# Kernel tuning notes

Measured on AMD Instinct MI355X. Metric: run time of the kernel, lower is better.

Reference implementation:

```python
import jax, jax.numpy as jnp
import numpy as np

D_MODEL = 1024
NUM_LAYERS = 4
VOCAB = 32000
NUM_HEADS = 8
HEAD_DIM = D_MODEL // NUM_HEADS
FFN_DIM = 2048
BATCH = 4
SEQ = 1024
LN_EPS = 1e-5
ROPE_THETA = 10000.0


def setup_inputs() -> dict:
    key = jax.random.key(0)
    ks = iter(jax.random.split(key, 32))
    std = 0.02
    L, D, H, Dh, F, V = NUM_LAYERS, D_MODEL, NUM_HEADS, HEAD_DIM, FFN_DIM, VOCAB
    inp = {
        "tokens": jax.random.randint(next(ks), (BATCH, SEQ), 0, V, dtype=jnp.int32),
        "emb": jax.random.normal(next(ks), (V, D), jnp.float32),
        # per-layer stacked params; Linear weights stored pre-transposed (in, out)
        "Wqkv": jax.random.normal(next(ks), (L, D, 3 * D), jnp.float32) * std,
        "bqkv": jnp.zeros((L, 3 * D), jnp.float32),
        "Wo": jax.random.normal(next(ks), (L, D, D), jnp.float32) * std,
        "bo": jnp.zeros((L, D), jnp.float32),
        "ln1_g": jnp.ones((L, D), jnp.float32),
        "ln1_b": jnp.zeros((L, D), jnp.float32),
        "ln2_g": jnp.ones((L, D), jnp.float32),
        "ln2_b": jnp.zeros((L, D), jnp.float32),
        "W1": jax.random.normal(next(ks), (L, D, F), jnp.float32) * std,
        "b1": jnp.zeros((L, F), jnp.float32),
        "W2": jax.random.normal(next(ks), (L, F, D), jnp.float32) * std,
        "b2": jnp.zeros((L, D), jnp.float32),
        "lnf_g": jnp.ones((D,), jnp.float32),
        "lnf_b": jnp.zeros((D,), jnp.float32),
        "Wout": jax.random.normal(next(ks), (D, V), jnp.float32) * std,
        "bout": jnp.zeros((V,), jnp.float32),
    }
    return inp


def _layernorm(x, g, b):
    mu = jnp.mean(x, -1, keepdims=True)
    var = jnp.mean(jnp.square(x - mu), -1, keepdims=True)
    return (x - mu) * jax.lax.rsqrt(var + LN_EPS) * g + b


def _rope_cos_sin(seq, dh, dtype):
    inv_freq = 1.0 / (ROPE_THETA ** (jnp.arange(0, dh, 2, dtype=jnp.float32) / dh))
    t = jnp.arange(seq, dtype=jnp.float32)
    freqs = jnp.outer(t, inv_freq)                      # [S, Dh/2]
    emb = jnp.concatenate([freqs, freqs], axis=-1)      # [S, Dh]
    return jnp.cos(emb).astype(dtype), jnp.sin(emb).astype(dtype)


def _rotate_half(x):
    x1, x2 = jnp.split(x, 2, axis=-1)
    return jnp.concatenate([-x2, x1], axis=-1)


def _apply_rope(x, cos, sin):
    # x: [B,S,H,Dh]; cos/sin: [S,Dh] -> broadcast over batch and heads
    return x * cos[None, :, None, :] + _rotate_half(x) * sin[None, :, None, :]


def reference(tokens, emb, Wqkv, bqkv, Wo, bo, ln1_g, ln1_b, ln2_g, ln2_b,
              W1, b1, W2, b2, lnf_g, lnf_b, Wout, bout):
    B, S = tokens.shape
    H, Dh = NUM_HEADS, HEAD_DIM
    x = emb[tokens]                                      # [B,S,D]
    cos, sin = _rope_cos_sin(S, Dh, x.dtype)
    causal = jnp.tril(jnp.ones((S, S), dtype=bool))      # True = keep
    scale = 1.0 / jnp.sqrt(jnp.asarray(Dh, x.dtype))

    def layer(xc, p):
        (wqkv, bq, wo, bo_, g1, b1_, g2, b2_, w1, bb1, w2, bb2) = p
        y = _layernorm(xc, g1, b1_)
        qkv = (y @ wqkv + bq).reshape(B, S, 3, H, Dh)
        q, k, v = qkv[:, :, 0], qkv[:, :, 1], qkv[:, :, 2]
        q = _apply_rope(q, cos, sin)
        k = _apply_rope(k, cos, sin)
        scores = jnp.einsum("bshd,bthd->bhst", q, k) * scale
        scores = jnp.where(causal[None, None], scores, -jnp.inf)
        attn = jax.nn.softmax(scores, axis=-1)
        ctx = jnp.einsum("bhst,bthd->bshd", attn, v).reshape(B, S, H * Dh)
        xc = xc + ctx @ wo + bo_
        z = _layernorm(xc, g2, b2_)
        ff = jax.nn.gelu(z @ w1 + bb1, approximate=False) @ w2 + bb2
        return xc + ff, None

    params = (Wqkv, bqkv, Wo, bo, ln1_g, ln1_b, ln2_g, ln2_b, W1, b1, W2, b2)
    x, _ = jax.lax.scan(layer, x, params)
    x = _layernorm(x, lnf_g, lnf_b)
    return x @ Wout + bout                                # [B,S,V]
```

## Files before the change

### kernel.cpp

```cpp
#include <hip/hip_runtime.h>
#include <hip/hip_bf16.h>
#include <math.h>


#define D_MODEL 1024
#define SEQ     1024
#define BATCH   4
#define NHEAD   8
#define HDIM    128
#define FFN     2048
#define NLAYER  4
#define VOCAB   32000
#define MROWS   (BATCH*SEQ)

typedef unsigned short ushort_t;
typedef __attribute__((ext_vector_type(8))) short s16x8;
typedef __attribute__((ext_vector_type(4))) float f32x4;

__device__ __forceinline__ ushort_t f2bf(float f) {
    union { float f; unsigned int u; } c; c.f = f;
    unsigned int u = c.u;
    unsigned int r = (u + 0x7FFFu + ((u >> 16) & 1u)) >> 16;
    return (ushort_t)r;
}
__device__ __forceinline__ float bf2f(ushort_t u) {
    union { unsigned int u; float f; } c; c.u = ((unsigned int)u) << 16; return c.f;
}

__device__ __forceinline__ void gload16(const void* g, void* l) {
    __builtin_amdgcn_global_load_lds(
        (const __attribute__((address_space(1))) unsigned int*)g,
        (__attribute__((address_space(3))) unsigned int*)l, 16, 0, 0);
}

__global__ __launch_bounds__(256) void embed_kernel(
    const int* __restrict__ tokens, const float* __restrict__ emb,
    float* __restrict__ X)
{
    int row = blockIdx.x;
    int t = tokens[row];
    const float4* src = (const float4*)(emb + (size_t)t * D_MODEL);
    float4* dst = (float4*)(X + (size_t)row * D_MODEL);
    dst[threadIdx.x] = src[threadIdx.x];
}

__global__ __launch_bounds__(256) void ln_kernel(
    const float* __restrict__ X, const float* __restrict__ g,
    const float* __restrict__ b, ushort_t* __restrict__ Y)
{
    __shared__ float red[8];
    int row = blockIdx.x;
    const float4* x4 = (const float4*)(X + (size_t)row * D_MODEL);
    float4 v = x4[threadIdx.x];
    float s  = v.x + v.y + v.z + v.w;
    float ss = v.x*v.x + v.y*v.y + v.z*v.z + v.w*v.w;
    #pragma unroll
    for (int o = 32; o > 0; o >>= 1) { s += __shfl_down(s, o); ss += __shfl_down(ss, o); }
    int wid = threadIdx.x >> 6;
    if ((threadIdx.x & 63) == 0) { red[wid] = s; red[wid + 4] = ss; }
    __syncthreads();
    float tot  = red[0] + red[1] + red[2] + red[3];
    float tot2 = red[4] + red[5] + red[6] + red[7];
    float mu  = tot * (1.0f / D_MODEL);
    float var = tot2 * (1.0f / D_MODEL) - mu * mu;
    float r = rsqrtf(var + 1e-5f);
    const float4* g4 = (const float4*)g;
    const float4* b4 = (const float4*)b;
    float4 gv = g4[threadIdx.x], bv = b4[threadIdx.x];
    ushort4 o;
    o.x = f2bf((v.x - mu) * r * gv.x + bv.x);
    o.y = f2bf((v.y - mu) * r * gv.y + bv.y);
    o.z = f2bf((v.z - mu) * r * gv.z + bv.z);
    o.w = f2bf((v.w - mu) * r * gv.w + bv.w);
    ((ushort4*)(Y + (size_t)row * D_MODEL))[threadIdx.x] = o;
}

__global__ __launch_bounds__(256) void wconv(
    const float* __restrict__ W, ushort_t* __restrict__ Wt, int K, int N)
{
    __shared__ float t[32][33];
    const float* Wl = W + (size_t)blockIdx.z * K * N;
    ushort_t* Wtl = Wt + (size_t)blockIdx.z * K * N;
    int k0 = blockIdx.y * 32, n0 = blockIdx.x * 32;
    int tid = threadIdx.x;
    int r = tid >> 3, c4 = (tid & 7) * 4;
    float4 v = *(const float4*)(Wl + (size_t)(k0 + r) * N + n0 + c4);
    t[r][c4+0] = v.x; t[r][c4+1] = v.y; t[r][c4+2] = v.z; t[r][c4+3] = v.w;
    __syncthreads();
    ushort4 o;
    o.x = f2bf(t[c4+0][r]); o.y = f2bf(t[c4+1][r]);
    o.z = f2bf(t[c4+2][r]); o.w = f2bf(t[c4+3][r]);
    *(ushort4*)(Wtl + (size_t)(n0 + r) * K + k0 + c4) = o;
}

__device__ __forceinline__ float gelu_exact(float x) {
    return 0.5f * x * (1.0f + erff(x * 0.70710678118654752f));
}

template<int ACT, int BETA, int OBF>
__global__ __launch_bounds__(256) void gemm_mfma(
    const ushort_t* __restrict__ A, const ushort_t* __restrict__ Bt,
    const float* __restrict__ bias, float* __restrict__ Cf,
    ushort_t* __restrict__ Cb, int M, int N, int K)
{
    __shared__ __align__(16) ushort_t As[128 * 32];
    __shared__ __align__(16) ushort_t Bs[128 * 32];
    int tid  = threadIdx.x;
    int lane = tid & 63, w = tid >> 6;
    int wr = w >> 1, wc = w & 1;
    int m0 = blockIdx.x * 128, n0 = blockIdx.y * 128;

    f32x4 acc[4][4] = {};

    const ushort_t* gA = A  + (size_t)(m0 + w * 32 + (lane >> 2)) * K + (lane & 3) * 8;
    const ushort_t* gB = Bt + (size_t)(n0 + w * 32 + (lane >> 2)) * K + (lane & 3) * 8;
    ushort_t* lA = As + w * 1024;
    ushort_t* lB = Bs + w * 1024;
    const size_t gstep16 = (size_t)16 * K;

    int lrow = lane & 15, kg = lane >> 4;
    const s16x8* pa = (const s16x8*)(As + (wr * 64 + lrow) * 32 + kg * 8);
    const s16x8* pb = (const s16x8*)(Bs + (wc * 64 + lrow) * 32 + kg * 8);

    for (int kt = 0; kt < K / 32; ++kt) {
        gload16(gA, lA);
        gload16(gA + gstep16, lA + 512);
        gload16(gB, lB);
        gload16(gB + gstep16, lB + 512);
        gA += 32; gB += 32;
        __syncthreads();
        s16x8 a[4], b[4];
        #pragma unroll
        for (int mi = 0; mi < 4; ++mi) a[mi] = pa[mi * 64];
        #pragma unroll
        for (int ni = 0; ni < 4; ++ni) b[ni] = pb[ni * 64];
        #pragma unroll
        for (int mi = 0; mi < 4; ++mi)
            #pragma unroll
            for (int ni = 0; ni < 4; ++ni)
                acc[mi][ni] = __builtin_amdgcn_mfma_f32_16x16x32_bf16(
                    a[mi], b[ni], acc[mi][ni], 0, 0, 0);
        __syncthreads();
    }

    #pragma unroll
    for (int mi = 0; mi < 4; ++mi) {
        int rbase = m0 + wr * 64 + mi * 16 + (lane >> 4) * 4;
        #pragma unroll
        for (int ni = 0; ni < 4; ++ni) {
            int col = n0 + wc * 64 + ni * 16 + (lane & 15);
            float bz = bias[col];
            f32x4 v = acc[mi][ni];
            #pragma unroll
            for (int j = 0; j < 4; ++j) {
                float x = v[j] + bz;
                if (ACT == 1) x = gelu_exact(x);
                size_t off = (size_t)(rbase + j) * N + col;
                if (OBF) {
                    Cb[off] = f2bf(x);
                } else {
                    if (BETA) x += Cf[off];
                    Cf[off] = x;
                }
            }
        }
    }
}

__global__ __launch_bounds__(64) void rope_table_kernel(float2* __restrict__ RT)
{
    int s = blockIdx.x, p = threadIdx.x;
    float inv = expf(-0.14391156831212788f * (float)p);
    float ang = (float)s * inv;
    float sn, c;
    sincosf(ang, &sn, &c);
    RT[s * 64 + p] = make_float2(c, sn);
}

__global__ __launch_bounds__(256) void ropeq_kernel(
    const ushort_t* __restrict__ QKVb, const float2* __restrict__ RT,
    ushort_t* __restrict__ Qb, ushort_t* __restrict__ Kb)
{
    int m = blockIdx.x;
    int b = m >> 10, s = m & (SEQ - 1);
    const ushort_t* rowbase = QKVb + (size_t)m * (3 * D_MODEL);
    const float2* t2 = RT + s * 64;
    int tid = threadIdx.x;
    int qk = tid >> 7;
    int rem = tid & 127;
    int hh = rem >> 4;
    int p4 = (rem & 15) * 4;
    const ushort_t* base = rowbase + qk * D_MODEL + hh * HDIM + p4;
    ushort4 lo = *(const ushort4*)base;
    ushort4 hi = *(const ushort4*)(base + 64);
    ushort_t lov[4] = {lo.x, lo.y, lo.z, lo.w};
    ushort_t hiv[4] = {hi.x, hi.y, hi.z, hi.w};
    ushort_t lor[4], hir[4];
    #pragma unroll
    for (int j = 0; j < 4; ++j) {
        float2 cs = t2[p4 + j];
        float x1 = bf2f(lov[j]), x2 = bf2f(hiv[j]);
        lor[j] = f2bf(x1 * cs.x - x2 * cs.y);
        hir[j] = f2bf(x2 * cs.x + x1 * cs.y);
    }
    ushort_t* dst = (qk ? Kb : Qb) + ((size_t)(b * NHEAD + hh) * SEQ + s) * HDIM + p4;
    *(ushort4*)dst        = make_ushort4(lor[0], lor[1], lor[2], lor[3]);
    *(ushort4*)(dst + 64) = make_ushort4(hir[0], hir[1], hir[2], hir[3]);
}

__global__ __launch_bounds__(256) void vtrans_kernel(
    const ushort_t* __restrict__ QKVb, ushort_t* __restrict__ Vt)
{
    __shared__ ushort_t tl[64][34];
    int s0 = blockIdx.x * 64;
    int d0 = blockIdx.y * 32;
    int b  = blockIdx.z;
    int tid = threadIdx.x;
    #pragma unroll
    for (int r = 0; r < 4; ++r) {
        int li = tid + r * 256;
        int row = li >> 4;
        int cp  = (li & 15) * 2;
        ushort2 v = *(const ushort2*)(QKVb + (size_t)(b * SEQ + s0 + row) * 3072
                                      + 2 * D_MODEL + d0 + cp);
        tl[row][cp]     = v.x;
        tl[row][cp + 1] = v.y;
    }
    __syncthreads();
    #pragma unroll
    for (int r = 0; r < 4; ++r) {
        int li = tid + r * 256;
        int drow = li >> 5;
        int sc   = (li & 31) * 2;
        ushort2 o;
        o.x = tl[sc][drow];
        o.y = tl[sc + 1][drow];
        *(ushort2*)(Vt + (size_t)(b * D_MODEL + d0 + drow) * SEQ + s0 + sc) = o;
    }
}

#define PSTR 72

__global__ __launch_bounds__(256) void attn_mfma(
    const ushort_t* __restrict__ Qb, const ushort_t* __restrict__ Kb,
    const ushort_t* __restrict__ Vt, ushort_t* __restrict__ Yb)
{
    __shared__ __align__(16) ushort_t Ks[64 * 136];
    __shared__ __align__(16) ushort_t Vts[128 * 72];
    __shared__ __align__(16) ushort_t Pl[4][16 * PSTR];
    int bid = blockIdx.x;
    int qt = bid & 15, h = (bid >> 4) & 7, b = bid >> 7;
    int q0 = qt * 64;
    int tid = threadIdx.x, lane = tid & 63, w = tid >> 6;
    int lr = lane & 15, g = lane >> 4;
    const float scale = 0.08838834764831845f;

    const ushort_t* Qbase = Qb + (size_t)((b * NHEAD + h) * SEQ) * HDIM;
    const ushort_t* Kbase = Kb + (size_t)((b * NHEAD + h) * SEQ) * HDIM;
    const ushort_t* Vbase = Vt + (size_t)(b * D_MODEL + h * HDIM) * SEQ;

    s16x8 aq[4];
    #pragma unroll
    for (int kc = 0; kc < 4; ++kc)
        aq[kc] = *(const s16x8*)(Qbase + (size_t)(q0 + w * 16 + lr) * HDIM + kc * 32 + g * 8);

    f32x4 acc_o[8] = {};
    float mx[4] = {-INFINITY, -INFINITY, -INFINITY, -INFINITY};
    float ls[4] = {};

    int ntiles = q0 / 64 + 1;
    for (int t = 0; t < ntiles; ++t) {
        int j0 = t * 64;
        __syncthreads();
        #pragma unroll
        for (int r = 0; r < 4; ++r) {
            int idx = tid + r * 256;
            int row = idx >> 4, c16 = idx & 15;
            *(s16x8*)&Ks[row * 136 + c16 * 8] =
                *(const s16x8*)(Kbase + (size_t)(j0 + row) * HDIM + c16 * 8);
        }
        #pragma unroll
        for (int r = 0; r < 4; ++r) {
            int idx = tid + r * 256;
            int row = idx >> 3, c8 = idx & 7;
            *(s16x8*)&Vts[row * 72 + c8 * 8] =
                *(const s16x8*)(Vbase + (size_t)row * SEQ + j0 + c8 * 8);
        }
        __syncthreads();

        f32x4 sa[4] = {};
        __builtin_amdgcn_s_setprio(1);
        #pragma unroll
        for (int nb = 0; nb < 4; ++nb)
            #pragma unroll
            for (int kc = 0; kc < 4; ++kc) {
                s16x8 bk = *(const s16x8*)&Ks[(nb * 16 + lr) * 136 + kc * 32 + g * 8];
                sa[nb] = __builtin_amdgcn_mfma_f32_16x16x32_bf16(aq[kc], bk, sa[nb], 0, 0, 0);
            }
        __builtin_amdgcn_s_setprio(0);

        bool diag = (j0 == q0);
        float pv[4][4];
        #pragma unroll
        for (int nb = 0; nb < 4; ++nb)
            #pragma unroll
            for (int j = 0; j < 4; ++j) {
                float v = sa[nb][j] * scale;
                if (diag) {
                    int kv = j0 + nb * 16 + lr;
                    int qq = q0 + w * 16 + g * 4 + j;
                    if (kv > qq) v = -INFINITY;
                }
                pv[nb][j] = v;
            }
        #pragma unroll
        for (int j = 0; j < 4; ++j) {
            float tm = fmaxf(fmaxf(pv[0][j], pv[1][j]), fmaxf(pv[2][j], pv[3][j]));
            #pragma unroll
            for (int o = 1; o < 16; o <<= 1) tm = fmaxf(tm, __shfl_xor(tm, o));
            float nm = fmaxf(mx[j], tm);
            float corr = expf(mx[j] - nm);
            float ts = 0.0f;
            #pragma unroll
            for (int nb = 0; nb < 4; ++nb) {
                float e = expf(pv[nb][j] - nm);
                pv[nb][j] = e;
                ts += e;
            }
            #pragma unroll
            for (int o = 1; o < 16; o <<= 1) ts += __shfl_xor(ts, o);
            ls[j] = ls[j] * corr + ts;
            mx[j] = nm;
            #pragma unroll
            for (int dn = 0; dn < 8; ++dn) acc_o[dn][j] *= corr;
        }
        #pragma unroll
        for (int nb = 0; nb < 4; ++nb)
            #pragma unroll
            for (int j = 0; j < 4; ++j)
                Pl[w][(g * 4 + j) * PSTR + nb * 16 + lr] = f2bf(pv[nb][j]);
        #pragma unroll
        for (int kk = 0; kk < 2; ++kk) {
            s16x8 pa = *(const s16x8*)&Pl[w][lr * PSTR + kk * 32 + g * 8];
            __builtin_amdgcn_s_setprio(1);
            #pragma unroll
            for (int dn = 0; dn < 8; ++dn) {
                s16x8 bv = *(const s16x8*)&Vts[(dn * 16 + lr) * 72 + kk * 32 + g * 8];
                acc_o[dn] = __builtin_amdgcn_mfma_f32_16x16x32_bf16(pa, bv, acc_o[dn], 0, 0, 0);
            }
            __builtin_amdgcn_s_setprio(0);
        }
    }

    float il[4];
    #pragma unroll
    for (int j = 0; j < 4; ++j) il[j] = 1.0f / ls[j];
    #pragma unroll
    for (int dn = 0; dn < 8; ++dn)
        #pragma unroll
        for (int j = 0; j < 4; ++j) {
            int q = q0 + w * 16 + g * 4 + j;
            Yb[(size_t)(b * SEQ + q) * D_MODEL + h * HDIM + dn * 16 + lr] =
                f2bf(acc_o[dn][j] * il[j]);
        }
}

extern "C" void kernel_launch(void* const* d_in, const int* in_sizes, int n_in,
                              void* d_out, int out_size, void* d_ws, size_t ws_size,
                              hipStream_t stream)
{
    const int*   tokens = (const int*)  d_in[0];
    const float* emb    = (const float*)d_in[1];
    const float* Wqkv   = (const float*)d_in[2];
    const float* bqkv   = (const float*)d_in[3];
    const float* Wo     = (const float*)d_in[4];
    const float* bo     = (const float*)d_in[5];
    const float* ln1_g  = (const float*)d_in[6];
    const float* ln1_b  = (const float*)d_in[7];
    const float* ln2_g  = (const float*)d_in[8];
    const float* ln2_b  = (const float*)d_in[9];
    const float* W1     = (const float*)d_in[10];
    const float* b1     = (const float*)d_in[11];
    const float* W2     = (const float*)d_in[12];
    const float* b2     = (const float*)d_in[13];
    const float* lnf_g  = (const float*)d_in[14];
    const float* lnf_b  = (const float*)d_in[15];
    const float* Wout   = (const float*)d_in[16];
    const float* bout   = (const float*)d_in[17];
    float* out = (float*)d_out;

    char* ws = (char*)d_ws;
    float*    X      = (float*)ws;
    ushort_t* Abuf   = (ushort_t*)(ws + 16777216);
    ushort_t* QKVb   = (ushort_t*)(ws + 25165824);
    ushort_t* Gbuf   = (ushort_t*)(ws + 25165824);
    ushort_t* Qbb    = (ushort_t*)(ws + 50331648);
    ushort_t* Kbb    = (ushort_t*)(ws + 58720256);
    ushort_t* Vtb    = (ushort_t*)(ws + 67108864);
    ushort_t* WqkvT  = (ushort_t*)(ws + 75497472);
    ushort_t* WoT    = (ushort_t*)(ws + 100663296);
    ushort_t* W1T    = (ushort_t*)(ws + 109051904);
    ushort_t* W2T    = (ushort_t*)(ws + 125829120);
    ushort_t* WoutT  = (ushort_t*)(ws + 142606336);
    float2*   RT     = (float2*)  (ws + 208142336);

    const int M = MROWS, Dm = D_MODEL, F = FFN, V = VOCAB;

    rope_table_kernel<<<SEQ, 64, 0, stream>>>(RT);

    wconv<<<dim3(3*Dm/32, Dm/32, NLAYER), 256, 0, stream>>>(Wqkv, WqkvT, Dm, 3*Dm);
    wconv<<<dim3(Dm/32,   Dm/32, NLAYER), 256, 0, stream>>>(Wo,   WoT,   Dm, Dm);
    wconv<<<dim3(F/32,    Dm/32, NLAYER), 256, 0, stream>>>(W1,   W1T,   Dm, F);
    wconv<<<dim3(Dm/32,   F/32,  NLAYER), 256, 0, stream>>>(W2,   W2T,   F,  Dm);
    wconv<<<dim3(V/32,    Dm/32, 1),      256, 0, stream>>>(Wout, WoutT, Dm, V);

    embed_kernel<<<MROWS, 256, 0, stream>>>(tokens, emb, X);

    for (int L = 0; L < NLAYER; ++L) {
        ln_kernel<<<MROWS, 256, 0, stream>>>(X, ln1_g + (size_t)L*Dm, ln1_b + (size_t)L*Dm, Abuf);
        gemm_mfma<0,0,1><<<dim3(M/128, 3*Dm/128), 256, 0, stream>>>(
            Abuf, WqkvT + (size_t)L*3*Dm*Dm, bqkv + (size_t)L*3*Dm, nullptr, QKVb, M, 3*Dm, Dm);
        ropeq_kernel<<<MROWS, 256, 0, stream>>>(QKVb, RT, Qbb, Kbb);
        vtrans_kernel<<<dim3(SEQ/64, Dm/32, BATCH), 256, 0, stream>>>(QKVb, Vtb);
        attn_mfma<<<BATCH*NHEAD*(SEQ/64), 256, 0, stream>>>(Qbb, Kbb, Vtb, Abuf);
        gemm_mfma<0,1,0><<<dim3(M/128, Dm/128), 256, 0, stream>>>(
            Abuf, WoT + (size_t)L*Dm*Dm, bo + (size_t)L*Dm, X, nullptr, M, Dm, Dm);
        ln_kernel<<<MROWS, 256, 0, stream>>>(X, ln2_g + (size_t)L*Dm, ln2_b + (size_t)L*Dm, Abuf);
        gemm_mfma<1,0,1><<<dim3(M/128, F/128), 256, 0, stream>>>(
            Abuf, W1T + (size_t)L*Dm*F, b1 + (size_t)L*F, nullptr, Gbuf, M, F, Dm);
        gemm_mfma<0,1,0><<<dim3(M/128, Dm/128), 256, 0, stream>>>(
            Gbuf, W2T + (size_t)L*F*Dm, b2 + (size_t)L*Dm, X, nullptr, M, Dm, F);
    }

    ln_kernel<<<MROWS, 256, 0, stream>>>(X, lnf_g, lnf_b, Abuf);
    gemm_mfma<0,0,0><<<dim3(M/128, V/128), 256, 0, stream>>>(
        Abuf, WoutT, bout, out, nullptr, M, V, Dm);
}
```

Baseline: 1.615 ms.

## Add 256x256-tile pipelined GEMM kernel for the vocab output projection

Adds a new 512-thread GEMM kernel with 256x256 output tiles, double-buffered LDS staging, and interleaved global prefetch across four MFMA sub-phases with raised wave priority. It replaces the 128x128 GEMM only for the final vocabulary projection (4096x32000x1024), the largest matmul in the model. Larger tiles raise arithmetic intensity and the finer load/compute interleave is meant to hide memory latency. In exchange it uses much more LDS per block and many accumulator registers, which lowers occupancy.

```diff
diff --git a/kernel.cpp b/kernel.cpp
--- a/kernel.cpp
+++ b/kernel.cpp
@@ -163,6 +163,150 @@
                     Cf[off] = x;
                 }
             }
+        }
+    }
+}
+
+__global__ __launch_bounds__(512) void gemm_big(
+    const ushort_t* __restrict__ A, const ushort_t* __restrict__ Bt,
+    const float* __restrict__ bias, float* __restrict__ C,
+    int M, int N, int K)
+{
+    __shared__ __align__(16) ushort_t As[2][256 * 64];
+    __shared__ __align__(16) ushort_t Bs[2][256 * 64];
+    int tid = threadIdx.x, lane = tid & 63, w = tid >> 6;
+    int wm = w >> 2, wn = w & 3;
+    int m0 = blockIdx.x * 256, n0 = blockIdx.y * 256;
+    int lr = lane & 15, kg = lane >> 4;
+    const int NKT = K / 64;
+
+    f32x4 acc[8][4] = {};
+
+    int srow = w * 8 + (lane >> 3);
+    int scol = (lane & 7) * 8;
+
+#define STAGE_A(db, ht, ktile) do { \
+    const ushort_t* s_ = A + (size_t)(m0 + (ht) * 128 + srow) * K + (size_t)(ktile) * 64 + scol; \
+    gload16(s_,                  &As[db][((ht) * 128 + w * 8) * 64]); \
+    gload16(s_ + (size_t)64 * K, &As[db][((ht) * 128 + 64 + w * 8) * 64]); \
+} while (0)
+#define STAGE_B(db, ht, ktile) do { \
+    const ushort_t* s_ = Bt + (size_t)(n0 + (ht) * 128 + srow) * K + (size_t)(ktile) * 64 + scol; \
+    gload16(s_,                  &Bs[db][((ht) * 128 + w * 8) * 64]); \
+    gload16(s_ + (size_t)64 * K, &Bs[db][((ht) * 128 + 64 + w * 8) * 64]); \
+} while (0)
+#define SBAR() do { __builtin_amdgcn_sched_barrier(0); \
+    __builtin_amdgcn_s_barrier(); __builtin_amdgcn_sched_barrier(0); } while (0)
+#define LGKM0() do { asm volatile("s_waitcnt lgkmcnt(0)" ::: "memory"); \
+    __builtin_amdgcn_sched_barrier(0); } while (0)
+
+    STAGE_A(0, 0, 0); STAGE_A(0, 1, 0); STAGE_B(0, 0, 0); STAGE_B(0, 1, 0);
+    STAGE_A(1, 0, 1);
+    asm volatile("s_waitcnt vmcnt(2)" ::: "memory");
+    SBAR();
+
+    for (int kt = 0; kt < NKT; ++kt) {
+        int d = kt & 1, dn = d ^ 1;
+        const ushort_t* pa = &As[d][(wm * 128 + lr) * 64 + kg * 8];
+        const ushort_t* pb = &Bs[d][(wn * 64  + lr) * 64 + kg * 8];
+        s16x8 a03[4][2], a47[4][2], b01[2][2], b23[2][2];
+
+        #pragma unroll
+        for (int mi = 0; mi < 4; ++mi) {
+            a03[mi][0] = *(const s16x8*)(pa + mi * 1024);
+            a03[mi][1] = *(const s16x8*)(pa + mi * 1024 + 32);
+        }
+        #pragma unroll
+        for (int ni = 0; ni < 2; ++ni) {
+            b01[ni][0] = *(const s16x8*)(pb + ni * 1024);
+            b01[ni][1] = *(const s16x8*)(pb + ni * 1024 + 32);
+        }
+        if (kt + 1 < NKT) STAGE_A(dn, 1, kt + 1);
+        LGKM0();
+        __builtin_amdgcn_s_setprio(1);
+        #pragma unroll
+        for (int mi = 0; mi < 4; ++mi)
+            #pragma unroll
+            for (int ni = 0; ni < 2; ++ni)
+                #pragma unroll
+                for (int kk = 0; kk < 2; ++kk)
+                    acc[mi][ni] = __builtin_amdgcn_mfma_f32_16x16x32_bf16(
+                        a03[mi][kk], b01[ni][kk], acc[mi][ni], 0, 0, 0);
+        __builtin_amdgcn_s_setprio(0);
+        SBAR();
+
+        #pragma unroll
+        for (int ni = 0; ni < 2; ++ni) {
+            b23[ni][0] = *(const s16x8*)(pb + (2 + ni) * 1024);
+            b23[ni][1] = *(const s16x8*)(pb + (2 + ni) * 1024 + 32);
+        }
+        if (kt + 1 < NKT) STAGE_B(dn, 0, kt + 1);
+        LGKM0();
+        __builtin_amdgcn_s_setprio(1);
+        #pragma unroll
+        for (int mi = 0; mi < 4; ++mi)
+            #pragma unroll
+            for (int ni = 0; ni < 2; ++ni)
+                #pragma unroll
+                for (int kk = 0; kk < 2; ++kk)
+                    acc[mi][2 + ni] = __builtin_amdgcn_mfma_f32_16x16x32_bf16(
+                        a03[mi][kk], b23[ni][kk], acc[mi][2 + ni], 0, 0, 0);
+        __builtin_amdgcn_s_setprio(0);
+        SBAR();
+
+        #pragma unroll
+        for (int mi = 0; mi < 4; ++mi) {
+            a47[mi][0] = *(const s16x8*)(pa + (4 + mi) * 1024);
+            a47[mi][1] = *(const s16x8*)(pa + (4 + mi) * 1024 + 32);
+        }
+        if (kt + 1 < NKT) STAGE_B(dn, 1, kt + 1);
+        LGKM0();
+        __builtin_amdgcn_s_setprio(1);
+        #pragma unroll
+        for (int mi = 0; mi < 4; ++mi)
+            #pragma unroll
+            for (int ni = 0; ni < 2; ++ni)
+                #pragma unroll
+                for (int kk = 0; kk < 2; ++kk)
+                    acc[4 + mi][ni] = __builtin_amdgcn_mfma_f32_16x16x32_bf16(
+                        a47[mi][kk], b01[ni][kk], acc[4 + mi][ni], 0, 0, 0);
+        __builtin_amdgcn_s_setprio(0);
+        SBAR();
+
+        if (kt + 2 < NKT) STAGE_A(d, 0, kt + 2);
+        __builtin_amdgcn_s_setprio(1);
+        #pragma unroll
+        for (int mi = 0; mi < 4; ++mi)
+            #pragma unroll
+            for (int ni = 0; ni < 2; ++ni)
+                #pragma unroll
+                for (int kk = 0; kk < 2; ++kk)
+                    acc[4 + mi][2 + ni] = __builtin_amdgcn_mfma_f32_16x16x32_bf16(
+                        a47[mi][kk], b23[ni][kk], acc[4 + mi][2 + ni], 0, 0, 0);
+        __builtin_amdgcn_s_setprio(0);
+        if (kt + 2 < NKT) {
+            asm volatile("s_waitcnt vmcnt(2)" ::: "memory");
+        } else {
+            asm volatile("s_waitcnt vmcnt(0)" ::: "memory");
+        }
+        SBAR();
+    }
+#undef STAGE_A
+#undef STAGE_B
+#undef SBAR
+#undef LGKM0
+
+    #pragma unroll
+    for (int mi = 0; mi < 8; ++mi) {
+        int rbase = m0 + wm * 128 + mi * 16 + kg * 4;
+        #pragma unroll
+        for (int ni = 0; ni < 4; ++ni) {
+            int col = n0 + wn * 64 + ni * 16 + lr;
+            float bz = bias[col];
+            f32x4 v = acc[mi][ni];
+            #pragma unroll
+            for (int j = 0; j < 4; ++j)
+                C[(size_t)(rbase + j) * N + col] = v[j] + bz;
         }
     }
 }
@@ -433,6 +577,6 @@
     }
 
     ln_kernel<<<MROWS, 256, 0, stream>>>(X, lnf_g, lnf_b, Abuf);
-    gemm_mfma<0,0,0><<<dim3(M/128, V/128), 256, 0, stream>>>(
-        Abuf, WoutT, bout, out, nullptr, M, V, Dm);
-}
+    gemm_big<<<dim3(M/256, V/256), 512, 0, stream>>>(
+        Abuf, WoutT, bout, out, M, V, Dm);
+}
```

New measurement: 1.607 ms. About the same (-0.4%).
